# Optimization experiments

Measured on AMD Instinct MI355X. Metric: run time of the kernel, lower is better.

## Reference

```python
import jax, jax.numpy as jnp
import numpy as np

H = 1536      # hidden_size
V = 128       # input_size == output_size (char vocab)
ML = 128      # MAX_LENGTH
SOS = 0


def setup_inputs() -> dict:
    key = jax.random.key(0)
    ks = jax.random.split(key, 16)
    s = 1.0 / np.sqrt(H)
    f = lambda k, shp: jax.random.uniform(k, shp, jnp.float32, -s, s)
    return {
        "input_tensor": jax.random.randint(ks[0], (64,), 0, V),
        "max_length": ML,
        # encoder params
        "emb_enc": f(ks[1], (V, H)),
        "enc_Wih": f(ks[2], (3 * H, H)),
        "enc_Whh": f(ks[3], (3 * H, H)),
        "enc_bih": f(ks[4], (3 * H,)),
        "enc_bhh": f(ks[5], (3 * H,)),
        # decoder params
        "emb_dec": f(ks[6], (V, H)),
        "attn_W": f(ks[7], (ML + 1, 2 * H)),
        "attn_b": f(ks[8], (ML + 1,)),
        "comb_W": f(ks[9], (H, 2 * H)),
        "comb_b": f(ks[10], (H,)),
        "dec_Wih": f(ks[11], (3 * H, H)),
        "dec_Whh": f(ks[12], (3 * H, H)),
        "dec_bih": f(ks[13], (3 * H,)),
        "dec_bhh": f(ks[14], (3 * H,)),
        "out_W": f(ks[15], (V, H)),
        "out_b": jnp.zeros((V,), jnp.float32),
    }


def gru_step(x, h, Wih, Whh, bih, bhh):
    # PyTorch GRUCell math
    gi = Wih @ x + bih
    gh = Whh @ h + bhh
    i_r, i_z, i_n = jnp.split(gi, 3)
    h_r, h_z, h_n = jnp.split(gh, 3)
    r = jax.nn.sigmoid(i_r + h_r)
    z = jax.nn.sigmoid(i_z + h_z)
    n = jnp.tanh(i_n + r * h_n)
    return (1.0 - z) * n + z * h


def reference(input_tensor, max_length, emb_enc, enc_Wih, enc_Whh, enc_bih,
              enc_bhh, emb_dec, attn_W, attn_b, comb_W, comb_b, dec_Wih,
              dec_Whh, dec_bih, dec_bhh, out_W, out_b):
    L = input_tensor.shape[0]

    # ---- encoder: sequential GRU over input tokens ----
    def enc_step(h, tok):
        h = gru_step(emb_enc[tok], h, enc_Wih, enc_Whh, enc_bih, enc_bhh)
        return h, h
    h0 = jnp.zeros((H,), emb_enc.dtype)
    enc_h, enc_outs = jax.lax.scan(enc_step, h0, input_tensor)  # (L, H)
    encoder_outputs = jnp.zeros((max_length + 1, H), emb_enc.dtype).at[:L].set(enc_outs)

    # ---- attention decoder: greedy decode for max_length steps ----
    def dec_step(carry, _):
        h, tok = carry
        emb = emb_dec[tok]                                   # (H,)
        attn_logits = attn_W @ jnp.concatenate([emb, h]) + attn_b
        attn_w = jax.nn.softmax(attn_logits)                 # (ML+1,)
        context = attn_w @ encoder_outputs                   # (H,)
        x = jax.nn.relu(comb_W @ jnp.concatenate([emb, context]) + comb_b)
        h = gru_step(x, h, dec_Wih, dec_Whh, dec_bih, dec_bhh)
        logp = jax.nn.log_softmax(out_W @ h + out_b)         # (V,)
        nxt = jnp.argmax(logp).astype(tok.dtype)
        return (h, nxt), (logp, nxt)

    tok0 = jnp.asarray(SOS, input_tensor.dtype)
    _, (logps, tokens) = jax.lax.scan(dec_step, (enc_h, tok0), None,
                                      length=max_length)
    return logps, tokens  # (ML, V) log-probs, (ML,) greedy token ids
```

## Files before the change

kernel.cpp:

```cpp
#include <hip/hip_runtime.h>
#include <math.h>

#define H     1536
#define H3    4608
#define V     128
#define ML    128
#define MLP1  129
#define LEN   64
#define NBLK  256
#define NTHR  384
#define WPB   6
#define NWAVE (NBLK*WPB)
#define ACC_N    260
#define ACC_ROWS 8
#define ACC_STEP (ACC_ROWS*ACC_N)
#define TA_STRIDE 132

#define SCALEF     1099511627776.0f
#define INV_SCALED 9.094947017729282379150390625e-13

#define OFF_BAR 0
#define OFF_ZB  4096
#define OFF_ACC 10240
#define OFF_HS  2156800
#define OFF_XS  2943232
#define OFF_XE  3729664
#define OFF_GI  4122880
#define OFF_EO  5302528
#define OFF_M   5695744
#define OFF_TA  6088960
#define OFF_TC  6156544
#define OFF_CT  6942976
#define WS_END  8540416
#define MEMSET_BYTES 2156800

__device__ __forceinline__ float uc_ldf(const float* p){
  return __hip_atomic_load(p, __ATOMIC_RELAXED, __HIP_MEMORY_SCOPE_AGENT);
}
__device__ __forceinline__ void uc_stf(float* p, float v){
  __hip_atomic_store(p, v, __ATOMIC_RELAXED, __HIP_MEMORY_SCOPE_AGENT);
}
__device__ __forceinline__ unsigned uc_ldu(const unsigned* p){
  return __hip_atomic_load(p, __ATOMIC_RELAXED, __HIP_MEMORY_SCOPE_AGENT);
}
__device__ __forceinline__ void uc_stu64(unsigned long long* p, unsigned long long v){
  __hip_atomic_store(p, v, __ATOMIC_RELAXED, __HIP_MEMORY_SCOPE_AGENT);
}

__device__ __forceinline__ float wred(float v){
  #pragma unroll
  for(int s=32;s>0;s>>=1) v += __shfl_xor(v, s, 64);
  return v;
}

__device__ __forceinline__ void load6(const float* p, int lane, float4 r[6]){
  const float4* q = (const float4*)p;
  #pragma unroll
  for(int c=0;c<6;c++) r[c] = q[c*64+lane];
}
__device__ __forceinline__ float dot4(const float4 a, const float4 b){
  return a.x*b.x + a.y*b.y + a.z*b.z + a.w*b.w;
}
__device__ __forceinline__ float dot6(const float4 a[6], const float4 b[6]){
  float s=0.f;
  #pragma unroll
  for(int c=0;c<6;c++) s += dot4(a[c], b[c]);
  return s;
}

__device__ __forceinline__ void gbar(unsigned* bar, int rnd){
  __syncthreads();
  if(threadIdx.x==0){
    unsigned* grp  = bar + 32*(1 + (blockIdx.x >> 4));
    unsigned* root = bar;
    unsigned a = __hip_atomic_fetch_add(grp, 1u, __ATOMIC_RELAXED, __HIP_MEMORY_SCOPE_AGENT);
    if((a & 0xFFFFu) == (unsigned)(16*rnd + 15)){
      unsigned ra = __hip_atomic_fetch_add(root, 1u, __ATOMIC_RELAXED, __HIP_MEMORY_SCOPE_AGENT);
      if(ra == (unsigned)(16*rnd + 15)){
        #pragma unroll
        for(int g=0; g<16; g++)
          __hip_atomic_fetch_add(bar + 32*(1+g), 0x10000u,
                                 __ATOMIC_RELAXED, __HIP_MEMORY_SCOPE_AGENT);
      } else {
        while((uc_ldu(grp) >> 16) < (unsigned)(rnd+1))
          __builtin_amdgcn_s_sleep(1);
      }
    } else {
      while((uc_ldu(grp) >> 16) < (unsigned)(rnd+1))
        __builtin_amdgcn_s_sleep(1);
    }
  }
  __syncthreads();
}

__global__ __launch_bounds__(NTHR, 2)
void seq2seq_kernel(const int* __restrict__ toks,
                    const float* __restrict__ emb_enc,
                    const float* __restrict__ enc_Wih,
                    const float* __restrict__ enc_Whh,
                    const float* __restrict__ enc_bih,
                    const float* __restrict__ enc_bhh,
                    const float* __restrict__ emb_dec,
                    const float* __restrict__ attn_W,
                    const float* __restrict__ attn_b,
                    const float* __restrict__ comb_W,
                    const float* __restrict__ comb_b,
                    const float* __restrict__ dec_Wih,
                    const float* __restrict__ dec_Whh,
                    const float* __restrict__ dec_bih,
                    const float* __restrict__ dec_bhh,
                    const float* __restrict__ out_W,
                    const float* __restrict__ out_b,
                    float* __restrict__ out,
                    char* __restrict__ ws)
{
  const int tid = threadIdx.x, b = blockIdx.x;
  const int lane = tid & 63, w = tid >> 6;
  const int gw = b*WPB + w;
  int rnd = 0;

  unsigned* bar = (unsigned*)ws;
  float* zb = (float*)(ws + OFF_ZB);
  unsigned long long* accseq = (unsigned long long*)(ws + OFF_ACC);
  float* hseq = (float*)(ws + OFF_HS);
  float* xseq = (float*)(ws + OFF_XS);
  float* Xe = (float*)(ws + OFF_XE);
  float* Gi = (float*)(ws + OFF_GI);
  float* EO = (float*)(ws + OFF_EO);
  float* Mm = (float*)(ws + OFF_M);
  float* tA = (float*)(ws + OFF_TA);
  float* tC = (float*)(ws + OFF_TC);
  float* cT = (float*)(ws + OFF_CT);

  __shared__ float smem[WPB*3*H];
  __shared__ float sh[H];
  __shared__ float sx[H];
  __shared__ float scT[WPB*ACC_N];
  __shared__ float sv[ACC_N];
  __shared__ float shc[8];

  for(int idx = b*NTHR + tid; idx < LEN*H; idx += NBLK*NTHR){
    int t = idx / H, k = idx - t*H;
    uc_stf(&Xe[idx], emb_enc[toks[t]*H + k]);
  }
  for(int idx = b*NTHR + tid; idx < H*257; idx += NBLK*NTHR){
    int i = idx / 257, c = idx - i*257;
    float v = (c < MLP1) ? attn_W[(size_t)c*2*H + H + i]
                         : out_W[(size_t)(c-MLP1)*H + i];
    uc_stf(&cT[(size_t)i*ACC_N + c], v);
  }
  gbar(bar, rnd++);

  {
    int r = b*18 + w*3;
    for(int g=0; g<4; g++){
      __syncthreads();
      for(int idx = tid; idx < 16*384; idx += NTHR)
        ((float4*)smem)[idx] = ((const float4*)Xe)[g*16*384 + idx];
      __syncthreads();
      float4 rv0[6], rv1[6], rv2[6];
      load6(enc_Wih + (size_t)r*H,     lane, rv0);
      load6(enc_Wih + (size_t)(r+1)*H, lane, rv1);
      load6(enc_Wih + (size_t)(r+2)*H, lane, rv2);
      float a0[16], a1[16], a2[16];
      #pragma unroll
      for(int t2=0;t2<16;t2++){ a0[t2]=0.f; a1[t2]=0.f; a2[t2]=0.f; }
      #pragma unroll
      for(int c=0;c<6;c++){
        #pragma unroll
        for(int t2=0;t2<16;t2++){
          float4 x = ((float4*)smem)[t2*384 + c*64 + lane];
          a0[t2] += dot4(rv0[c], x);
          a1[t2] += dot4(rv1[c], x);
          a2[t2] += dot4(rv2[c], x);
        }
      }
      float bi0 = enc_bih[r], bi1 = enc_bih[r+1], bi2 = enc_bih[r+2];
      #pragma unroll
      for(int t2=0;t2<16;t2++){
        float s0 = wred(a0[t2]), s1 = wred(a1[t2]), s2 = wred(a2[t2]);
        if(lane==0){
          uc_stf(&Gi[(size_t)(g*16+t2)*H3 + r    ], s0 + bi0);
          uc_stf(&Gi[(size_t)(g*16+t2)*H3 + r + 1], s1 + bi1);
          uc_stf(&Gi[(size_t)(g*16+t2)*H3 + r + 2], s2 + bi2);
        }
      }
    }
  }
  gbar(bar, rnd++);

  {
    int i = gw;
    float4 rv[6]; load6(comb_W + (size_t)i*2*H, lane, rv);
    for(int g=0; g<8; g++){
      __syncthreads();
      for(int idx = tid; idx < 16*384; idx += NTHR)
        ((float4*)smem)[idx] = ((const float4*)emb_dec)[g*16*384 + idx];
      __syncthreads();
      float a0[16];
      #pragma unroll
      for(int t2=0;t2<16;t2++) a0[t2]=0.f;
      #pragma unroll
      for(int c=0;c<6;c++){
        #pragma unroll
        for(int t2=0;t2<16;t2++){
          float4 x = ((float4*)smem)[t2*384 + c*64 + lane];
          a0[t2] += dot4(rv[c], x);
        }
      }
      #pragma unroll
      for(int t2=0;t2<16;t2++){
        float s = wred(a0[t2]);
        if(lane==0) uc_stf(&tC[(size_t)(g*16+t2)*H + i], s);
      }
    }
  }

  for(int task = gw; task < MLP1*V; task += NWAVE){
    int j = task >> 7, v = task & 127;
    float4 av[6]; load6(attn_W + (size_t)j*2*H, lane, av);
    float4 ev[6]; load6(emb_dec + (size_t)v*H, lane, ev);
    float s = wred(dot6(av, ev));
    if(lane==0) uc_stf(&tA[v*TA_STRIDE + j], s);
  }
  gbar(bar, rnd++);

  for(int idx = tid; idx < 18*384; idx += NTHR){
    int row = idx/384, k4 = idx - row*384;
    int w2 = row/3, gate = row - w2*3;
    ((float4*)smem)[idx] =
      ((const float4*)enc_Whh)[((size_t)gate*H + b*WPB + w2)*384 + k4];
  }
  const int i0 = gw;
  float gi0 = Gi[(size_t)lane*H3 + i0];
  float gi1 = Gi[(size_t)lane*H3 + i0 + H];
  float gi2 = Gi[(size_t)lane*H3 + i0 + 2*H];
  float eb0 = enc_bhh[i0], eb1 = enc_bhh[i0+H], eb2 = enc_bhh[i0+2*H];
  __syncthreads();

  for(int t=0; t<LEN; t++){
    const float* hprev = (t==0) ? zb : (EO + (size_t)(t-1)*H);
    ((float4*)sh)[tid] = ((const float4*)hprev)[tid];
    __syncthreads();
    float4 hv[6]; load6(sh, lane, hv);
    float s[3];
    #pragma unroll
    for(int g=0; g<3; g++){
      const float4* sr = (const float4*)smem + (w*3+g)*384;
      float t0=0.f;
      #pragma unroll
      for(int c=0;c<6;c++) t0 += dot4(sr[c*64+lane], hv[c]);
      s[g] = wred(t0);
    }
    float ir = __shfl(gi0, t, 64), iz = __shfl(gi1, t, 64), in_ = __shfl(gi2, t, 64);
    if(lane==0){
      float r = 1.f/(1.f+expf(-(ir + s[0] + eb0)));
      float z = 1.f/(1.f+expf(-(iz + s[1] + eb1)));
      float n = tanhf(in_ + r*(s[2] + eb2));
      float hn = (1.f-z)*n + z*sh[i0];
      uc_stf(&EO[(size_t)t*H + i0], hn);
    }
    gbar(bar, rnd++);
  }

  {
    int i = gw;
    float4 rv[6]; load6(comb_W + (size_t)i*2*H + H, lane, rv);
    for(int g=0; g<4; g++){
      __syncthreads();
      for(int idx = tid; idx < 16*384; idx += NTHR)
        ((float4*)smem)[idx] = ((const float4*)EO)[g*16*384 + idx];
      __syncthreads();
      float a0[16];
      #pragma unroll
      for(int t2=0;t2<16;t2++) a0[t2]=0.f;
      #pragma unroll
      for(int c=0;c<6;c++){
        #pragma unroll
        for(int t2=0;t2<16;t2++){
          float4 x = ((float4*)smem)[t2*384 + c*64 + lane];
          a0[t2] += dot4(rv[c], x);
        }
      }
      #pragma unroll
      for(int t2=0;t2<16;t2++){
        float s = wred(a0[t2]);
        if(lane==0) uc_stf(&Mm[(size_t)i*64 + g*16 + t2], s);
      }
    }
  }

  if(gw < MLP1){
    int j = gw;
    float4 av[6]; load6(attn_W + (size_t)j*2*H + H, lane, av);
    float4 hv[6]; load6(EO + (size_t)(LEN-1)*H, lane, hv);
    float s = wred(dot6(av, hv));
    if(lane==0)
      uc_stu64(&accseq[j], (unsigned long long)(long long)rintf(s*SCALEF));
  }
  for(int idx = tid; idx < 18*384; idx += NTHR){
    int row = idx/384, k4 = idx - row*384;
    int w2 = row/3, gate = row - w2*3;
    ((float4*)smem)[idx] =
      ((const float4*)dec_Whh)[((size_t)gate*H + b*WPB + w2)*384 + k4];
  }
  for(int idx = tid; idx < WPB*ACC_N; idx += NTHR){
    int w2 = idx / ACC_N, c = idx - w2*ACC_N;
    scT[idx] = cT[(size_t)(b*WPB + w2)*ACC_N + c];
  }
  gbar(bar, rnd++);

  const int i = gw;
  float4 wx0[6], wx1[6], wx2[6];
  load6(dec_Wih + (size_t)i*H,         lane, wx0);
  load6(dec_Wih + ((size_t)H + i)*H,   lane, wx1);
  load6(dec_Wih + ((size_t)2*H + i)*H, lane, wx2);
  const float mreg = Mm[(size_t)i*64 + lane];
  const float ct0 = tC[(size_t)lane*H + i];
  const float ct1 = tC[(size_t)(64+lane)*H + i];
  const float ib0 = dec_bih[i], ib1 = dec_bih[i+H], ib2 = dec_bih[i+2*H];
  const float hb0 = dec_bhh[i], hb1 = dec_bhh[i+H], hb2 = dec_bhh[i+2*H];
  const float cb  = comb_b[i];
  const float ob0 = out_b[lane], ob1 = out_b[64+lane];
  const float ab0 = attn_b[lane], ab1 = attn_b[64+lane], ab2 = attn_b[128];

  for(int t=0; t<ML; t++){
    const float* hprev = (t==0) ? (EO + (size_t)(LEN-1)*H) : (hseq + (size_t)(t-1)*H);
    const unsigned long long* accC = accseq + (size_t)t*ACC_STEP;
    unsigned long long* accA = accseq + (size_t)(t+1)*ACC_STEP;

    ((float4*)sh)[tid] = ((const float4*)hprev)[tid];
    if(tid < 257){
      long long s = 0;
      #pragma unroll
      for(int r2=0; r2<ACC_ROWS; r2++)
        s += ((const long long*)accC)[r2*ACC_N + tid];
      sv[tid] = (float)((double)s * INV_SCALED);
    }
    __syncthreads();

    float4 hv[6]; load6(sh, lane, hv);
    float sWh[3];
    #pragma unroll
    for(int g=0; g<3; g++){
      const float4* sp = (const float4*)smem + (w*3+g)*384;
      float t1=0.f;
      #pragma unroll
      for(int c=0;c<6;c++) t1 += dot4(sp[c*64+lane], hv[c]);
      sWh[g] = wred(t1);
    }

    float o0 = sv[MLP1+lane]    + ob0;
    float o1 = sv[MLP1+64+lane] + ob1;
    float mv; int mi;
    if(o0 >= o1){ mv=o0; mi=lane; } else { mv=o1; mi=64+lane; }
    #pragma unroll
    for(int sft=32; sft>0; sft>>=1){
      float ov = __shfl_xor(mv, sft, 64);
      int   oi = __shfl_xor(mi, sft, 64);
      if(ov > mv || (ov == mv && oi < mi)){ mv = ov; mi = oi; }
    }
    const int tok = (t==0) ? 0 : mi;
    if(b==0 && w==0 && t>0){
      float e0w = expf(o0-mv) + expf(o1-mv);
      float ss = wred(e0w);
      float lse = mv + logf(ss);
      out[(size_t)(t-1)*V + lane]      = o0 - lse;
      out[(size_t)(t-1)*V + 64 + lane] = o1 - lse;
      if(lane==0) out[(size_t)ML*V + (t-1)] = (float)tok;
    }

    float v0 = sv[lane]      + tA[tok*TA_STRIDE + lane]      + ab0;
    float v1 = sv[64+lane]   + tA[tok*TA_STRIDE + 64 + lane] + ab1;
    float v2 = (lane==0) ? (sv[128] + tA[tok*TA_STRIDE + 128] + ab2) : -1e30f;
    float m0 = fmaxf(fmaxf(v0, v1), v2);
    #pragma unroll
    for(int sft=32; sft>0; sft>>=1) m0 = fmaxf(m0, __shfl_xor(m0, sft, 64));
    float e0 = expf(v0 - m0);
    float esum = e0 + expf(v1 - m0) + ((lane==0) ? expf(v2 - m0) : 0.f);
    esum = wred(esum);
    const float invd = 1.f/esum;

    {
      float s = wred(mreg * e0);
      float ctv = (tok < 64) ? __shfl(ct0, tok, 64) : __shfl(ct1, tok-64, 64);
      if(lane==0)
        uc_stf(&xseq[(size_t)t*H + i], fmaxf(ctv + s*invd + cb, 0.f));
    }
    gbar(bar, rnd++);

    ((float4*)sx)[tid] = ((const float4*)(xseq + (size_t)t*H))[tid];
    __syncthreads();
    float4 xv[6]; load6(sx, lane, xv);
    float t0=0.f, t1=0.f, t2=0.f;
    #pragma unroll
    for(int c=0;c<6;c++){
      t0 += dot4(wx0[c], xv[c]);
      t1 += dot4(wx1[c], xv[c]);
      t2 += dot4(wx2[c], xv[c]);
    }
    float sWx0 = wred(t0), sWx1 = wred(t1), sWx2 = wred(t2);
    if(lane==0){
      float r = 1.f/(1.f+expf(-(sWx0+ib0 + sWh[0]+hb0)));
      float z = 1.f/(1.f+expf(-(sWx1+ib1 + sWh[1]+hb1)));
      float n = tanhf(sWx2+ib2 + r*(sWh[2]+hb2));
      float hn = (1.f-z)*n + z*sh[i];
      uc_stf(&hseq[(size_t)t*H + i], hn);
      shc[w] = hn;
    }
    __syncthreads();
    if(tid < 257){
      float s = 0.f;
      #pragma unroll
      for(int w2=0; w2<WPB; w2++)
        s += scT[w2*ACC_N + tid] * shc[w2];
      atomicAdd(&accA[(b & (ACC_ROWS-1))*ACC_N + tid],
                (unsigned long long)(long long)rintf(s*SCALEF));
    }
    gbar(bar, rnd++);
  }

  if(b==0){
    const unsigned long long* accC = accseq + (size_t)ML*ACC_STEP;
    if(tid < 257){
      long long s = 0;
      #pragma unroll
      for(int r2=0; r2<ACC_ROWS; r2++)
        s += ((const long long*)accC)[r2*ACC_N + tid];
      sv[tid] = (float)((double)s * INV_SCALED);
    }
    __syncthreads();
    if(w==0){
      float o0 = sv[MLP1+lane]    + ob0;
      float o1 = sv[MLP1+64+lane] + ob1;
      float mv; int mi;
      if(o0 >= o1){ mv=o0; mi=lane; } else { mv=o1; mi=64+lane; }
      #pragma unroll
      for(int sft=32; sft>0; sft>>=1){
        float ov = __shfl_xor(mv, sft, 64);
        int   oi = __shfl_xor(mi, sft, 64);
        if(ov > mv || (ov == mv && oi < mi)){ mv = ov; mi = oi; }
      }
      float e0 = expf(o0-mv) + expf(o1-mv);
      float ss = wred(e0);
      float lse = mv + logf(ss);
      out[(size_t)(ML-1)*V + lane]      = o0 - lse;
      out[(size_t)(ML-1)*V + 64 + lane] = o1 - lse;
      if(lane==0) out[(size_t)ML*V + (ML-1)] = (float)mi;
    }
  }
}

extern "C" void kernel_launch(void* const* d_in, const int* in_sizes, int n_in,
                              void* d_out, int out_size, void* d_ws, size_t ws_size,
                              hipStream_t stream){
  (void)in_sizes; (void)n_in; (void)out_size; (void)ws_size;
  const int*   toks    = (const int*)  d_in[0];
  const float* emb_enc = (const float*)d_in[2];
  const float* enc_Wih = (const float*)d_in[3];
  const float* enc_Whh = (const float*)d_in[4];
  const float* enc_bih = (const float*)d_in[5];
  const float* enc_bhh = (const float*)d_in[6];
  const float* emb_dec = (const float*)d_in[7];
  const float* attn_W  = (const float*)d_in[8];
  const float* attn_b  = (const float*)d_in[9];
  const float* comb_W  = (const float*)d_in[10];
  const float* comb_b  = (const float*)d_in[11];
  const float* dec_Wih = (const float*)d_in[12];
  const float* dec_Whh = (const float*)d_in[13];
  const float* dec_bih = (const float*)d_in[14];
  const float* dec_bhh = (const float*)d_in[15];
  const float* out_W   = (const float*)d_in[16];
  const float* out_b   = (const float*)d_in[17];
  float* outp = (float*)d_out;
  char*  ws   = (char*)d_ws;

  hipMemsetAsync(d_ws, 0, MEMSET_BYTES, stream);

  void* args[] = { &toks, &emb_enc, &enc_Wih, &enc_Whh, &enc_bih, &enc_bhh,
                   &emb_dec, &attn_W, &attn_b, &comb_W, &comb_b,
                   &dec_Wih, &dec_Whh, &dec_bih, &dec_bhh, &out_W, &out_b,
                   &outp, &ws };
  hipLaunchCooperativeKernel((void*)seq2seq_kernel, dim3(NBLK), dim3(NTHR),
                             args, 0, stream);
}
```

Baseline: 2.289 ms.

## Replace grid barriers with tagged-value flag polling in encoder and decoder loops

Grid-wide barriers in the encoder GRU loop and the decoder step loop are replaced by per-element publish/poll. Each value is stored as a 64-bit word carrying its step tag, and consumers spin on exactly the values they need, using double-buffered hidden and input vectors. The accumulator hand-off uses sharded arrival counters in place of a full barrier. This aims to cut barrier latency on the serial critical path, at the cost of more polling traffic and subtler memory-ordering correctness.

```diff
diff --git a/kernel.cpp b/kernel.cpp
--- a/kernel.cpp
+++ b/kernel.cpp
@@ -20,19 +20,20 @@
 #define INV_SCALED 9.094947017729282379150390625e-13
 
 #define OFF_BAR 0
-#define OFF_ZB  4096
-#define OFF_ACC 10240
-#define OFF_HS  2156800
-#define OFF_XS  2943232
-#define OFF_XE  3729664
-#define OFF_GI  4122880
-#define OFF_EO  5302528
-#define OFF_M   5695744
-#define OFF_TA  6088960
-#define OFF_TC  6156544
-#define OFF_CT  6942976
-#define WS_END  8540416
-#define MEMSET_BYTES 2156800
+#define OFF_ACC 4096
+#define OFF_EH  2150656
+#define OFF_HC  2175232
+#define OFF_XC  2199808
+#define OFF_CNT 2224384
+#define MEMSET_BYTES 2226432
+#define OFF_XE  2226432
+#define OFF_GI  2619648
+#define OFF_EO  3799296
+#define OFF_M   4192512
+#define OFF_TA  4585728
+#define OFF_TC  4653312
+#define OFF_CT  5439744
+#define WS_END  7037184
 
 __device__ __forceinline__ float uc_ldf(const float* p){
   return __hip_atomic_load(p, __ATOMIC_RELAXED, __HIP_MEMORY_SCOPE_AGENT);
@@ -43,8 +44,31 @@
 __device__ __forceinline__ unsigned uc_ldu(const unsigned* p){
   return __hip_atomic_load(p, __ATOMIC_RELAXED, __HIP_MEMORY_SCOPE_AGENT);
 }
+__device__ __forceinline__ unsigned long long uc_ld64(const unsigned long long* p){
+  return __hip_atomic_load(p, __ATOMIC_RELAXED, __HIP_MEMORY_SCOPE_AGENT);
+}
 __device__ __forceinline__ void uc_stu64(unsigned long long* p, unsigned long long v){
   __hip_atomic_store(p, v, __ATOMIC_RELAXED, __HIP_MEMORY_SCOPE_AGENT);
+}
+
+__device__ __forceinline__ void pub(unsigned long long* p, float v, unsigned tag){
+  uc_stu64(p, ((unsigned long long)tag << 32) | (unsigned long long)__float_as_uint(v));
+}
+__device__ __forceinline__ void poll4(const unsigned long long* base, unsigned tag,
+                                      float* dst){
+  bool g0=false,g1=false,g2=false,g3=false;
+  for(;;){
+    if(!g0){ unsigned long long r=uc_ld64(base+0);
+      if((unsigned)(r>>32)==tag){ dst[0]=__uint_as_float((unsigned)r); g0=true; } }
+    if(!g1){ unsigned long long r=uc_ld64(base+1);
+      if((unsigned)(r>>32)==tag){ dst[1]=__uint_as_float((unsigned)r); g1=true; } }
+    if(!g2){ unsigned long long r=uc_ld64(base+2);
+      if((unsigned)(r>>32)==tag){ dst[2]=__uint_as_float((unsigned)r); g2=true; } }
+    if(!g3){ unsigned long long r=uc_ld64(base+3);
+      if((unsigned)(r>>32)==tag){ dst[3]=__uint_as_float((unsigned)r); g3=true; } }
+    if(g0&&g1&&g2&&g3) break;
+    __builtin_amdgcn_s_sleep(1);
+  }
 }
 
 __device__ __forceinline__ float wred(float v){
@@ -120,10 +144,11 @@
   int rnd = 0;
 
   unsigned* bar = (unsigned*)ws;
-  float* zb = (float*)(ws + OFF_ZB);
   unsigned long long* accseq = (unsigned long long*)(ws + OFF_ACC);
-  float* hseq = (float*)(ws + OFF_HS);
-  float* xseq = (float*)(ws + OFF_XS);
+  unsigned long long* eh  = (unsigned long long*)(ws + OFF_EH);
+  unsigned long long* hc  = (unsigned long long*)(ws + OFF_HC);
+  unsigned long long* xc  = (unsigned long long*)(ws + OFF_XC);
+  unsigned* cnt = (unsigned*)(ws + OFF_CNT);
   float* Xe = (float*)(ws + OFF_XE);
   float* Gi = (float*)(ws + OFF_GI);
   float* EO = (float*)(ws + OFF_EO);
@@ -239,10 +264,14 @@
   __syncthreads();
 
   for(int t=0; t<LEN; t++){
-    const float* hprev = (t==0) ? zb : (EO + (size_t)(t-1)*H);
-    ((float4*)sh)[tid] = ((const float4*)hprev)[tid];
+    if(t==0){
+      sh[4*tid]=0.f; sh[4*tid+1]=0.f; sh[4*tid+2]=0.f; sh[4*tid+3]=0.f;
+    } else {
+      poll4(eh + (size_t)((t-1)&1)*H + 4*tid, (unsigned)t, &sh[4*tid]);
+    }
     __syncthreads();
     float4 hv[6]; load6(sh, lane, hv);
+    const float hp = sh[i0];
     float s[3];
     #pragma unroll
     for(int g=0; g<3; g++){
@@ -257,11 +286,12 @@
       float r = 1.f/(1.f+expf(-(ir + s[0] + eb0)));
       float z = 1.f/(1.f+expf(-(iz + s[1] + eb1)));
       float n = tanhf(in_ + r*(s[2] + eb2));
-      float hn = (1.f-z)*n + z*sh[i0];
+      float hn = (1.f-z)*n + z*hp;
+      pub(&eh[(size_t)(t&1)*H + i0], hn, (unsigned)(t+1));
       uc_stf(&EO[(size_t)t*H + i0], hn);
     }
-    gbar(bar, rnd++);
-  }
+  }
+  gbar(bar, rnd++);
 
   {
     int i = gw;
@@ -325,21 +355,30 @@
   const float ab0 = attn_b[lane], ab1 = attn_b[64+lane], ab2 = attn_b[128];
 
   for(int t=0; t<ML; t++){
-    const float* hprev = (t==0) ? (EO + (size_t)(LEN-1)*H) : (hseq + (size_t)(t-1)*H);
     const unsigned long long* accC = accseq + (size_t)t*ACC_STEP;
     unsigned long long* accA = accseq + (size_t)(t+1)*ACC_STEP;
 
-    ((float4*)sh)[tid] = ((const float4*)hprev)[tid];
+    if(t==0){
+      ((float4*)sh)[tid] = ((const float4*)(EO + (size_t)(LEN-1)*H))[tid];
+    } else {
+      poll4(hc + (size_t)((t-1)&1)*H + 4*tid, (unsigned)t, &sh[4*tid]);
+      if(tid < 16){
+        const unsigned* cl = cnt + tid*32;
+        while(uc_ldu(cl) < (unsigned)(16*t)) __builtin_amdgcn_s_sleep(1);
+      }
+    }
+    __syncthreads();
+
     if(tid < 257){
       long long s = 0;
       #pragma unroll
       for(int r2=0; r2<ACC_ROWS; r2++)
-        s += ((const long long*)accC)[r2*ACC_N + tid];
+        s += (long long)uc_ld64(&accC[r2*ACC_N + tid]);
       sv[tid] = (float)((double)s * INV_SCALED);
     }
-    __syncthreads();
 
     float4 hv[6]; load6(sh, lane, hv);
+    const float hp = sh[i];
     float sWh[3];
     #pragma unroll
     for(int g=0; g<3; g++){
@@ -349,6 +388,7 @@
       for(int c=0;c<6;c++) t1 += dot4(sp[c*64+lane], hv[c]);
       sWh[g] = wred(t1);
     }
+    __syncthreads();
 
     float o0 = sv[MLP1+lane]    + ob0;
     float o1 = sv[MLP1+64+lane] + ob1;
@@ -385,12 +425,13 @@
       float s = wred(mreg * e0);
       float ctv = (tok < 64) ? __shfl(ct0, tok, 64) : __shfl(ct1, tok-64, 64);
       if(lane==0)
-        uc_stf(&xseq[(size_t)t*H + i], fmaxf(ctv + s*invd + cb, 0.f));
-    }
-    gbar(bar, rnd++);
-
-    ((float4*)sx)[tid] = ((const float4*)(xseq + (size_t)t*H))[tid];
-    __syncthreads();
+        pub(&xc[(size_t)(t&1)*H + i], fmaxf(ctv + s*invd + cb, 0.f),
+            (unsigned)(t+1));
+    }
+
+    poll4(xc + (size_t)(t&1)*H + 4*tid, (unsigned)(t+1), &sx[4*tid]);
+    __syncthreads();
+
     float4 xv[6]; load6(sx, lane, xv);
     float t0=0.f, t1=0.f, t2=0.f;
     #pragma unroll
@@ -404,11 +445,12 @@
       float r = 1.f/(1.f+expf(-(sWx0+ib0 + sWh[0]+hb0)));
       float z = 1.f/(1.f+expf(-(sWx1+ib1 + sWh[1]+hb1)));
       float n = tanhf(sWx2+ib2 + r*(sWh[2]+hb2));
-      float hn = (1.f-z)*n + z*sh[i];
-      uc_stf(&hseq[(size_t)t*H + i], hn);
+      float hn = (1.f-z)*n + z*hp;
+      pub(&hc[(size_t)(t&1)*H + i], hn, (unsigned)(t+1));
       shc[w] = hn;
     }
     __syncthreads();
+
     if(tid < 257){
       float s = 0.f;
       #pragma unroll
@@ -417,16 +459,25 @@
       atomicAdd(&accA[(b & (ACC_ROWS-1))*ACC_N + tid],
                 (unsigned long long)(long long)rintf(s*SCALEF));
     }
-    gbar(bar, rnd++);
+    asm volatile("s_waitcnt vmcnt(0)" ::: "memory");
+    __syncthreads();
+    if(tid==0)
+      __hip_atomic_fetch_add(cnt + (b>>4)*32, 1u,
+                             __ATOMIC_RELAXED, __HIP_MEMORY_SCOPE_AGENT);
   }
 
   if(b==0){
+    if(tid < 16){
+      const unsigned* cl = cnt + tid*32;
+      while(uc_ldu(cl) < (unsigned)(16*ML)) __builtin_amdgcn_s_sleep(1);
+    }
+    __syncthreads();
     const unsigned long long* accC = accseq + (size_t)ML*ACC_STEP;
     if(tid < 257){
       long long s = 0;
       #pragma unroll
       for(int r2=0; r2<ACC_ROWS; r2++)
-        s += ((const long long*)accC)[r2*ACC_N + tid];
+        s += (long long)uc_ld64(&accC[r2*ACC_N + tid]);
       sv[tid] = (float)((double)s * INV_SCALED);
     }
     __syncthreads();
```

After: 2.571 ms. +12.3%, slower.

## Replace grid barriers with per-channel monotonic counters and overlap Whh matvec with accumulator wait

Applied to the files above, without the earlier changes.

Swaps the global grid barriers in the encoder and decoder loops for per-channel arrival counters spread over 16 cache lines. Each block bumps its counter and waits only on the data it needs next (encoder h, decoder x, decoder h, accumulator). The recurrent Whh matvec is moved ahead of the wait on the attention/output accumulator so the two overlap. The log-softmax output is now computed once at the end, spread across blocks, instead of on the critical path. This cuts barrier latency but relies on careful memory ordering with relaxed atomics.

```diff
diff --git a/kernel.cpp b/kernel.cpp
--- a/kernel.cpp
+++ b/kernel.cpp
@@ -19,24 +19,26 @@
 #define SCALEF     1099511627776.0f
 #define INV_SCALED 9.094947017729282379150390625e-13
 
+#define CH_ENC 0
+#define CH_EX  1
+#define CH_EH  2
+#define CH_EA  3
+
 #define OFF_BAR 0
-#define OFF_ZB  4096
-#define OFF_ACC 10240
-#define OFF_HS  2156800
-#define OFF_XS  2943232
-#define OFF_XE  3729664
-#define OFF_GI  4122880
-#define OFF_EO  5302528
-#define OFF_M   5695744
-#define OFF_TA  6088960
-#define OFF_TC  6156544
-#define OFF_CT  6942976
-#define WS_END  8540416
-#define MEMSET_BYTES 2156800
-
-__device__ __forceinline__ float uc_ldf(const float* p){
-  return __hip_atomic_load(p, __ATOMIC_RELAXED, __HIP_MEMORY_SCOPE_AGENT);
-}
+#define OFF_CNT 4096
+#define OFF_ACC 8192
+#define MEMSET_BYTES 2154752
+#define OFF_HS  2154752
+#define OFF_XS  2941184
+#define OFF_XE  3727616
+#define OFF_GI  4120832
+#define OFF_EO  5300480
+#define OFF_M   5693696
+#define OFF_TA  6086912
+#define OFF_TC  6154496
+#define OFF_CT  6940928
+#define WS_END  8538368
+
 __device__ __forceinline__ void uc_stf(float* p, float v){
   __hip_atomic_store(p, v, __ATOMIC_RELAXED, __HIP_MEMORY_SCOPE_AGENT);
 }
@@ -45,6 +47,18 @@
 }
 __device__ __forceinline__ void uc_stu64(unsigned long long* p, unsigned long long v){
   __hip_atomic_store(p, v, __ATOMIC_RELAXED, __HIP_MEMORY_SCOPE_AGENT);
+}
+
+__device__ __forceinline__ void bump(unsigned* cnt, int ch, int b){
+  __hip_atomic_fetch_add(cnt + (ch*16 + (b>>4))*16, 1u,
+                         __ATOMIC_RELAXED, __HIP_MEMORY_SCOPE_AGENT);
+}
+__device__ __forceinline__ void waitline(const unsigned* cnt, int ch, int tid,
+                                         unsigned target){
+  if(tid < 16){
+    const unsigned* line = cnt + (ch*16 + tid)*16;
+    while(uc_ldu(line) < target) __builtin_amdgcn_s_sleep(1);
+  }
 }
 
 __device__ __forceinline__ float wred(float v){
@@ -120,7 +134,7 @@
   int rnd = 0;
 
   unsigned* bar = (unsigned*)ws;
-  float* zb = (float*)(ws + OFF_ZB);
+  unsigned* cnt = (unsigned*)(ws + OFF_CNT);
   unsigned long long* accseq = (unsigned long long*)(ws + OFF_ACC);
   float* hseq = (float*)(ws + OFF_HS);
   float* xseq = (float*)(ws + OFF_XS);
@@ -239,10 +253,17 @@
   __syncthreads();
 
   for(int t=0; t<LEN; t++){
-    const float* hprev = (t==0) ? zb : (EO + (size_t)(t-1)*H);
-    ((float4*)sh)[tid] = ((const float4*)hprev)[tid];
+    if(t==0){
+      float4 z4 = {0.f,0.f,0.f,0.f};
+      ((float4*)sh)[tid] = z4;
+    } else {
+      waitline(cnt, CH_ENC, tid, (unsigned)(16*t));
+      __syncthreads();
+      ((float4*)sh)[tid] = ((const float4*)(EO + (size_t)(t-1)*H))[tid];
+    }
     __syncthreads();
     float4 hv[6]; load6(sh, lane, hv);
+    const float hp = sh[i0];
     float s[3];
     #pragma unroll
     for(int g=0; g<3; g++){
@@ -257,11 +278,14 @@
       float r = 1.f/(1.f+expf(-(ir + s[0] + eb0)));
       float z = 1.f/(1.f+expf(-(iz + s[1] + eb1)));
       float n = tanhf(in_ + r*(s[2] + eb2));
-      float hn = (1.f-z)*n + z*sh[i0];
+      float hn = (1.f-z)*n + z*hp;
       uc_stf(&EO[(size_t)t*H + i0], hn);
     }
-    gbar(bar, rnd++);
-  }
+    __syncthreads();
+    if(tid==0) bump(cnt, CH_ENC, b);
+  }
+  waitline(cnt, CH_ENC, tid, (unsigned)(16*LEN));
+  __syncthreads();
 
   {
     int i = gw;
@@ -325,11 +349,32 @@
   const float ab0 = attn_b[lane], ab1 = attn_b[64+lane], ab2 = attn_b[128];
 
   for(int t=0; t<ML; t++){
-    const float* hprev = (t==0) ? (EO + (size_t)(LEN-1)*H) : (hseq + (size_t)(t-1)*H);
     const unsigned long long* accC = accseq + (size_t)t*ACC_STEP;
     unsigned long long* accA = accseq + (size_t)(t+1)*ACC_STEP;
 
-    ((float4*)sh)[tid] = ((const float4*)hprev)[tid];
+    if(t==0){
+      ((float4*)sh)[tid] = ((const float4*)(EO + (size_t)(LEN-1)*H))[tid];
+    } else {
+      waitline(cnt, CH_EH, tid, (unsigned)(16*t));
+      __syncthreads();
+      ((float4*)sh)[tid] = ((const float4*)(hseq + (size_t)(t-1)*H))[tid];
+    }
+    __syncthreads();
+
+    float4 hv[6]; load6(sh, lane, hv);
+    const float hp = sh[i];
+    float sWh[3];
+    #pragma unroll
+    for(int g=0; g<3; g++){
+      const float4* sp = (const float4*)smem + (w*3+g)*384;
+      float t1=0.f;
+      #pragma unroll
+      for(int c=0;c<6;c++) t1 += dot4(sp[c*64+lane], hv[c]);
+      sWh[g] = wred(t1);
+    }
+
+    if(t>0) waitline(cnt, CH_EA, tid, (unsigned)(16*t));
+    __syncthreads();
     if(tid < 257){
       long long s = 0;
       #pragma unroll
@@ -338,17 +383,6 @@
       sv[tid] = (float)((double)s * INV_SCALED);
     }
     __syncthreads();
-
-    float4 hv[6]; load6(sh, lane, hv);
-    float sWh[3];
-    #pragma unroll
-    for(int g=0; g<3; g++){
-      const float4* sp = (const float4*)smem + (w*3+g)*384;
-      float t1=0.f;
-      #pragma unroll
-      for(int c=0;c<6;c++) t1 += dot4(sp[c*64+lane], hv[c]);
-      sWh[g] = wred(t1);
-    }
 
     float o0 = sv[MLP1+lane]    + ob0;
     float o1 = sv[MLP1+64+lane] + ob1;
@@ -361,14 +395,6 @@
       if(ov > mv || (ov == mv && oi < mi)){ mv = ov; mi = oi; }
     }
     const int tok = (t==0) ? 0 : mi;
-    if(b==0 && w==0 && t>0){
-      float e0w = expf(o0-mv) + expf(o1-mv);
-      float ss = wred(e0w);
-      float lse = mv + logf(ss);
-      out[(size_t)(t-1)*V + lane]      = o0 - lse;
-      out[(size_t)(t-1)*V + 64 + lane] = o1 - lse;
-      if(lane==0) out[(size_t)ML*V + (t-1)] = (float)tok;
-    }
 
     float v0 = sv[lane]      + tA[tok*TA_STRIDE + lane]      + ab0;
     float v1 = sv[64+lane]   + tA[tok*TA_STRIDE + 64 + lane] + ab1;
@@ -387,8 +413,11 @@
       if(lane==0)
         uc_stf(&xseq[(size_t)t*H + i], fmaxf(ctv + s*invd + cb, 0.f));
     }
-    gbar(bar, rnd++);
-
+    __syncthreads();
+    if(tid==0) bump(cnt, CH_EX, b);
+
+    waitline(cnt, CH_EX, tid, (unsigned)(16*(t+1)));
+    __syncthreads();
     ((float4*)sx)[tid] = ((const float4*)(xseq + (size_t)t*H))[tid];
     __syncthreads();
     float4 xv[6]; load6(sx, lane, xv);
@@ -404,11 +433,13 @@
       float r = 1.f/(1.f+expf(-(sWx0+ib0 + sWh[0]+hb0)));
       float z = 1.f/(1.f+expf(-(sWx1+ib1 + sWh[1]+hb1)));
       float n = tanhf(sWx2+ib2 + r*(sWh[2]+hb2));
-      float hn = (1.f-z)*n + z*sh[i];
+      float hn = (1.f-z)*n + z*hp;
       uc_stf(&hseq[(size_t)t*H + i], hn);
       shc[w] = hn;
     }
     __syncthreads();
+    if(tid==0) bump(cnt, CH_EH, b);
+
     if(tid < 257){
       float s = 0.f;
       #pragma unroll
@@ -417,37 +448,36 @@
       atomicAdd(&accA[(b & (ACC_ROWS-1))*ACC_N + tid],
                 (unsigned long long)(long long)rintf(s*SCALEF));
     }
-    gbar(bar, rnd++);
-  }
-
-  if(b==0){
-    const unsigned long long* accC = accseq + (size_t)ML*ACC_STEP;
-    if(tid < 257){
-      long long s = 0;
-      #pragma unroll
-      for(int r2=0; r2<ACC_ROWS; r2++)
-        s += ((const long long*)accC)[r2*ACC_N + tid];
-      sv[tid] = (float)((double)s * INV_SCALED);
-    }
-    __syncthreads();
-    if(w==0){
-      float o0 = sv[MLP1+lane]    + ob0;
-      float o1 = sv[MLP1+64+lane] + ob1;
-      float mv; int mi;
-      if(o0 >= o1){ mv=o0; mi=lane; } else { mv=o1; mi=64+lane; }
-      #pragma unroll
-      for(int sft=32; sft>0; sft>>=1){
-        float ov = __shfl_xor(mv, sft, 64);
-        int   oi = __shfl_xor(mi, sft, 64);
-        if(ov > mv || (ov == mv && oi < mi)){ mv = ov; mi = oi; }
-      }
-      float e0 = expf(o0-mv) + expf(o1-mv);
-      float ss = wred(e0);
-      float lse = mv + logf(ss);
-      out[(size_t)(ML-1)*V + lane]      = o0 - lse;
-      out[(size_t)(ML-1)*V + 64 + lane] = o1 - lse;
-      if(lane==0) out[(size_t)ML*V + (ML-1)] = (float)mi;
-    }
+    __syncthreads();
+    if(tid==0) bump(cnt, CH_EA, b);
+  }
+
+  waitline(cnt, CH_EA, tid, (unsigned)(16*ML));
+  __syncthreads();
+  if(b < ML && w == 0){
+    const unsigned long long* accC = accseq + (size_t)(b+1)*ACC_STEP;
+    long long s0 = 0, s1 = 0;
+    #pragma unroll
+    for(int r2=0; r2<ACC_ROWS; r2++){
+      s0 += ((const long long*)accC)[r2*ACC_N + MLP1 + lane];
+      s1 += ((const long long*)accC)[r2*ACC_N + MLP1 + 64 + lane];
+    }
+    float o0 = (float)((double)s0 * INV_SCALED) + ob0;
+    float o1 = (float)((double)s1 * INV_SCALED) + ob1;
+    float mv; int mi;
+    if(o0 >= o1){ mv=o0; mi=lane; } else { mv=o1; mi=64+lane; }
+    #pragma unroll
+    for(int sft=32; sft>0; sft>>=1){
+      float ov = __shfl_xor(mv, sft, 64);
+      int   oi = __shfl_xor(mi, sft, 64);
+      if(ov > mv || (ov == mv && oi < mi)){ mv = ov; mi = oi; }
+    }
+    float e0 = expf(o0-mv) + expf(o1-mv);
+    float ss = wred(e0);
+    float lse = mv + logf(ss);
+    out[(size_t)b*V + lane]      = o0 - lse;
+    out[(size_t)b*V + 64 + lane] = o1 - lse;
+    if(lane==0) out[(size_t)ML*V + b] = (float)mi;
   }
 }
 
```

After: 2.040 ms. 10.9% less time.
